# Optimization experiments

Hardware: AMD Instinct MI355X
Metric: run time of the kernel (lower is better)

Reference implementation:

```python
import jax, jax.numpy as jnp
import numpy as np

N, D_IN, D_EMB, K = 16384, 1024, 256, 1024
ALPHA, EPS = 0.01, 1e-5


def setup_inputs() -> dict:
    key = jax.random.key(0)
    ks = jax.random.split(key, 6)
    inp = jax.random.normal(ks[0], (N, D_IN), dtype=jnp.float32)
    W_send = jax.random.normal(ks[1], (D_IN, D_EMB), dtype=jnp.float32) / np.sqrt(D_IN)
    b_send = jnp.zeros((D_EMB,), dtype=jnp.float32)
    W_recv = jax.random.normal(ks[2], (D_EMB, D_IN), dtype=jnp.float32) / np.sqrt(D_EMB)
    b_recv = jnp.zeros((D_IN,), dtype=jnp.float32)
    codebook = jax.random.normal(ks[3], (K, D_EMB), dtype=jnp.float32)
    ema_vecs = codebook.copy()
    ema_size = jnp.zeros((K,), dtype=jnp.float32)
    return {"input": inp, "W_send": W_send, "b_send": b_send,
            "W_recv": W_recv, "b_recv": b_recv, "codebook": codebook,
            "ema_vecs": ema_vecs, "ema_size": ema_size}


def reference(input, W_send, b_send, W_recv, b_recv, codebook, ema_vecs, ema_size):
    sg = jax.lax.stop_gradient
    # send projection -> latent z  [N, D_EMB]
    z = input @ W_send + b_send
    # nearest-neighbor lookup: argmin_k ||e_k||^2 - 2 <z, e_k>
    sqr = jnp.sum(codebook * codebook, axis=1)          # [K]
    cov = jnp.einsum('nj,kj->nk', z, codebook)          # [N, K]
    codes = jnp.argmin(sqr - 2.0 * cov, axis=-1)        # [N] int
    # fetch embeddings (gather)
    vectors = codebook[codes]                            # [N, D_EMB]
    # mse losses, reduction='sum'
    embedding = jnp.sum((vectors - sg(z)) ** 2)
    commitment = jnp.sum((z - sg(vectors)) ** 2)
    # straight-through output
    emb_out = z + sg(vectors - z)
    # EMA accumulate (one-hot scatter == segment_sum)
    upd_vecs = jax.ops.segment_sum(z, codes, num_segments=K)              # [K, D_EMB]
    upd_size = jax.ops.segment_sum(jnp.ones((z.shape[0],), z.dtype), codes, num_segments=K)
    ema_vecs_new = ema_vecs + ALPHA * (upd_vecs - ema_vecs)
    ema_size_new = ema_size + ALPHA * (upd_size - ema_size)
    # EMA update (Laplace-smoothed centroid)
    n = jnp.sum(ema_size_new)
    coef = n / (n + K * EPS)
    size = coef * (ema_size_new + EPS)
    weight_new = ema_vecs_new / size[:, None]
    # empirical entropy of the codes in bits
    prob = jnp.bincount(codes, length=K).astype(jnp.float32) / codes.size
    ent = -jnp.sum(jnp.where(prob > 0, prob * jnp.log(prob), 0.0)) / jnp.log(2.0)
    # recv projection
    x = emb_out @ W_recv + b_recv
    return (x, codes, embedding, commitment, ent, ema_vecs_new, ema_size_new, weight_new)
```

## Files before the change

kernel.cpp:

```cpp
#include <hip/hip_runtime.h>
#include <math.h>

#define NROWS 16384
#define DIN   1024
#define DEMB  256
#define KC    1024
#define ALPHA 0.01f
#define EPSV  1e-5f
#define INV2048 4.8828125e-4f
#define CHUNK 32
#define COV_CHUNKS 8

typedef _Float16 f16;
typedef __attribute__((ext_vector_type(4)))  _Float16 f16x4;
typedef __attribute__((ext_vector_type(8)))  _Float16 f16x8;
typedef __attribute__((ext_vector_type(16))) float    f32x16;
typedef unsigned long long u64;

#define OFF_Z       0
#define OFF_R       4194304
#define OFF_SQR     5242880
#define OFF_ZH      5243904
#define OFF_ZL      7341056
#define OFF_WTH     9438208
#define OFF_WTL     9569280
#define OFF_CBH     9700352
#define OFF_CBL     9831424
#define OFF_KEYS    9962496
#define OFF_CODES   9995264
#define OFF_LIST    10011648
#define OFF_OFFS    10028032
#define OFF_UPD     10029056
#define OFF_HIST    10291200
#define OFF_CURSOR  10292224
#define OFF_LOSS    10293248
#define OFF_COUNTSF 10293264
#define OFF_SIZE    10294288

#define OUT_X      0
#define OUT_CODES  16777216
#define OUT_EMB    16793600
#define OUT_COMMIT 16793601
#define OUT_ENT    16793602
#define OUT_EMAV   16793603
#define OUT_EMAS   17055747
#define OUT_W      17056771

__device__ __forceinline__ void split_f32(float x, f16& h, f16& l) {
    h = (f16)x;
    l = (f16)((x - (float)h) * 2048.0f);
}

__global__ __launch_bounds__(256) void prep_kernel(const float* __restrict__ W_send,
                                                   const float* __restrict__ W_recv,
                                                   const float* __restrict__ cb,
                                                   float* __restrict__ ws) {
    const int b = blockIdx.x;
    const int t = threadIdx.x;
    int* wsi = (int*)ws;

    if (b < 256) {
        f16* wth = (f16*)(ws + OFF_WTH);
        f16* wtl = (f16*)(ws + OFF_WTL);
        const int n = b;
        f16x4 h4, l4;
#pragma unroll
        for (int j = 0; j < 4; ++j) {
            int k = t * 4 + j;
            float x = W_send[(size_t)k * DEMB + n];
            f16 h, l; split_f32(x, h, l);
            h4[j] = h; l4[j] = l;
        }
        *(f16x4*)&wth[(size_t)n * DIN + t * 4] = h4;
        *(f16x4*)&wtl[(size_t)n * DIN + t * 4] = l4;
    } else if (b < 512) {
        f16* cbh = (f16*)(ws + OFF_CBH);
        f16* cbl = (f16*)(ws + OFF_CBL);
        int idx = ((b - 256) * 256 + t) * 4;
        float4 v = *(const float4*)&cb[idx];
        f16x4 h4, l4;
        f16 h, l;
        split_f32(v.x, h, l); h4[0] = h; l4[0] = l;
        split_f32(v.y, h, l); h4[1] = h; l4[1] = l;
        split_f32(v.z, h, l); h4[2] = h; l4[2] = l;
        split_f32(v.w, h, l); h4[3] = h; l4[3] = l;
        *(f16x4*)&cbh[idx] = h4;
        *(f16x4*)&cbl[idx] = l4;
    } else if (b < 768) {
        f16* wrh = (f16*)(ws + OFF_ZH);
        f16* wrl = (f16*)(ws + OFF_ZH + 131072);
        const int n = (b - 512) * 4 + (t >> 6);
        const int lane = t & 63;
        f16x4 h4, l4;
#pragma unroll
        for (int j = 0; j < 4; ++j) {
            int k = lane * 4 + j;
            float x = W_recv[(size_t)k * DIN + n];
            f16 h, l; split_f32(x, h, l);
            h4[j] = h; l4[j] = l;
        }
        *(f16x4*)&wrh[(size_t)n * DEMB + lane * 4] = h4;
        *(f16x4*)&wrl[(size_t)n * DEMB + lane * 4] = l4;
    } else if (b < 1024) {
        float* sqr = ws + OFF_SQR;
        const int k = (b - 768) * 4 + (t >> 6);
        const int lane = t & 63;
        float4 v = ((const float4*)cb)[k * 64 + lane];
        float s = v.x * v.x + v.y * v.y + v.z * v.z + v.w * v.w;
        for (int off = 32; off > 0; off >>= 1) s += __shfl_down(s, off, 64);
        if (lane == 0) sqr[k] = s;
    } else if (b < 1280) {
        float4 zed = make_float4(0.f, 0.f, 0.f, 0.f);
        *(float4*)&ws[OFF_UPD + (size_t)(b - 1024) * 1024 + t * 4] = zed;
    } else if (b == 1280) {
#pragma unroll
        for (int j = 0; j < 4; ++j) {
            wsi[OFF_HIST + t * 4 + j] = 0;
            wsi[OFF_CURSOR + t * 4 + j] = 0;
        }
        if (t < 16) ws[OFF_LOSS + t] = 0.f;
    } else {
        u64* keys = (u64*)(ws + OFF_KEYS);
        keys[(b - 1281) * 256 + t] = ~0ull;
    }
}

__global__ __launch_bounds__(512) void gemm1_mfma(const float* __restrict__ in,
                                                  const f16* __restrict__ wth,
                                                  const f16* __restrict__ wtl,
                                                  const float* __restrict__ bsend,
                                                  float* __restrict__ z,
                                                  f16* __restrict__ zh,
                                                  f16* __restrict__ zl) {
    __shared__ f16 sm[2 * 2 * 2 * 128 * 64];
    const int tid = threadIdx.x;
    const int wave = tid >> 6, lane = tid & 63;
    const int half = lane >> 5, l31 = lane & 31;
    const int wrow = wave >> 2, wcol = wave & 3;

    const int L = blockIdx.x;
    const int v = L >> 3;
    const int bx = v & 1;
    const int by = (L & 7) + 8 * (v >> 1);
    const int rowBase = by * 128;
    const int colBase = bx * 128;

    const int sr  = tid >> 2;
    const int skq = tid & 3;
    const int sr7 = sr & 7;

    f32x16 accm[2] = {};
    f32x16 accx[2] = {};

    auto stageB = [&](int buf, int ks) {
#pragma unroll
        for (int i = 0; i < 4; ++i) {
            const int q  = wave * 4 + i;
            const int hl = q >> 4;
            const int c  = (q & 15) * 8 + (lane >> 3);
            const int p  = lane & 7;
            const int s  = p ^ (c & 7);
            const f16* src = (hl ? wtl : wth)
                           + (size_t)(colBase + c) * DIN + ks + s * 8;
            f16* dst = sm + buf * 32768 + 16384 + q * 512 + lane * 8;
            __builtin_amdgcn_global_load_lds(
                (const __attribute__((address_space(1))) void*)src,
                (__attribute__((address_space(3))) void*)dst, 16, 0, 0);
        }
    };

    auto loadA = [&](int ks, float4* av) {
        const float* src = &in[(size_t)(rowBase + sr) * DIN + ks + skq * 16];
#pragma unroll
        for (int j = 0; j < 4; ++j) av[j] = ((const float4*)src)[j];
    };

    auto writeA = [&](int buf, const float4* av) {
        f16* Abase = sm + buf * 32768;
#pragma unroll
        for (int q = 0; q < 2; ++q) {
            f16x8 h8, l8;
#pragma unroll
            for (int j = 0; j < 2; ++j) {
                float4 v4 = av[q * 2 + j];
                f16 h, l;
                split_f32(v4.x, h, l); h8[j * 4 + 0] = h; l8[j * 4 + 0] = l;
                split_f32(v4.y, h, l); h8[j * 4 + 1] = h; l8[j * 4 + 1] = l;
                split_f32(v4.z, h, l); h8[j * 4 + 2] = h; l8[j * 4 + 2] = l;
                split_f32(v4.w, h, l); h8[j * 4 + 3] = h; l8[j * 4 + 3] = l;
            }
            const int s = skq * 2 + q;
            const int off = sr * 64 + ((s ^ sr7) << 3);
            *(f16x8*)&Abase[off] = h8;
            *(f16x8*)&Abase[8192 + off] = l8;
        }
    };

    auto compute = [&](int buf) {
        const f16* Ah = sm + buf * 32768;
        const f16* Al = Ah + 8192;
        const f16* Bh = Ah + 16384;
        const f16* Bl = Ah + 24576;
        const int c  = wcol * 32 + l31;
        const int c7 = c & 7;
#pragma unroll
        for (int t4 = 0; t4 < 4; ++t4) {
            const int s = t4 * 2 + half;
            f16x8 a_h[2], a_l[2];
#pragma unroll
            for (int rt = 0; rt < 2; ++rt) {
                const int r = wrow * 64 + rt * 32 + l31;
                const int off = r * 64 + ((s ^ (r & 7)) << 3);
                a_h[rt] = *(const f16x8*)&Ah[off];
                a_l[rt] = *(const f16x8*)&Al[off];
            }
            const int boff = c * 64 + ((s ^ c7) << 3);
            f16x8 b_h = *(const f16x8*)&Bh[boff];
            f16x8 b_l = *(const f16x8*)&Bl[boff];
#pragma unroll
            for (int rt = 0; rt < 2; ++rt) {
                accm[rt] = __builtin_amdgcn_mfma_f32_32x32x16_f16(a_h[rt], b_h, accm[rt], 0, 0, 0);
                accx[rt] = __builtin_amdgcn_mfma_f32_32x32x16_f16(a_h[rt], b_l, accx[rt], 0, 0, 0);
                accx[rt] = __builtin_amdgcn_mfma_f32_32x32x16_f16(a_l[rt], b_h, accx[rt], 0, 0, 0);
            }
        }
    };

    stageB(0, 0);
    {
        float4 av[4];
        loadA(0, av);
        writeA(0, av);
    }
    __syncthreads();

    int cur = 0;
    for (int step = 0; step < 16; ++step) {
        float4 av[4];
        const bool pf = (step + 1) < 16;
        if (pf) {
            stageB(cur ^ 1, (step + 1) * 64);
            loadA((step + 1) * 64, av);
        }
        compute(cur);
        if (pf) writeA(cur ^ 1, av);
        __syncthreads();
        cur ^= 1;
    }

#pragma unroll
    for (int rt = 0; rt < 2; ++rt) {
        const int col = colBase + wcol * 32 + l31;
        const float bb = bsend[col];
#pragma unroll
        for (int reg = 0; reg < 16; ++reg) {
            const int row = rowBase + wrow * 64 + rt * 32 + (reg & 3) + 8 * (reg >> 2) + 4 * half;
            const float zv = accm[rt][reg] + INV2048 * accx[rt][reg] + bb;
            const size_t o = (size_t)row * DEMB + col;
            z[o] = zv;
            f16 h = (f16)zv;
            zh[o] = h;
            zl[o] = (f16)((zv - (float)h) * 2048.0f);
        }
    }
}

__global__ __launch_bounds__(256, 2) void gemm2_mfma(const f16* __restrict__ cbh,
                                                     const f16* __restrict__ cbl,
                                                     const f16* __restrict__ wrh,
                                                     const f16* __restrict__ wrl,
                                                     float* __restrict__ R) {
    __shared__ f16 sm[16384];
    const int tid = threadIdx.x;
    const int wave = tid >> 6, lane = tid & 63;
    const int half = lane >> 5, l31 = lane & 31;
    const int wr = wave >> 1, wc = wave & 1;
    const int rowBase = blockIdx.y * 64;
    const int colBase = blockIdx.x * 64;

    f32x16 accm = {}, accx = {};

    for (int step = 0; step < 4; ++step) {
        const int ks = step * 64;
        __syncthreads();
#pragma unroll
        for (int i = 0; i < 8; ++i) {
            const int q   = wave * 8 + i;
            const int arr = q >> 3;
            const int grp = q & 7;
            const int r   = grp * 8 + (lane >> 3);
            const int p   = lane & 7;
            const int s   = p ^ (r & 7);
            const f16* basep = (arr == 0) ? cbh : (arr == 1) ? cbl
                             : (arr == 2) ? wrh : wrl;
            const int rowg = ((arr >= 2) ? colBase : rowBase) + r;
            const f16* src = basep + (size_t)rowg * DEMB + ks + s * 8;
            f16* dst = sm + arr * 4096 + grp * 512;
            __builtin_amdgcn_global_load_lds(
                (const __attribute__((address_space(1))) void*)src,
                (__attribute__((address_space(3))) void*)dst, 16, 0, 0);
        }
        __syncthreads();
#pragma unroll
        for (int t = 0; t < 4; ++t) {
            const int sgi = t * 2 + half;
            const int ar = wr * 32 + l31;
            const int bc = wc * 32 + l31;
            const int aoff = ar * 64 + ((sgi ^ (ar & 7)) << 3);
            const int boff = bc * 64 + ((sgi ^ (bc & 7)) << 3);
            f16x8 a_h = *(const f16x8*)&sm[aoff];
            f16x8 a_l = *(const f16x8*)&sm[4096 + aoff];
            f16x8 b_h = *(const f16x8*)&sm[8192 + boff];
            f16x8 b_l = *(const f16x8*)&sm[12288 + boff];
            accm = __builtin_amdgcn_mfma_f32_32x32x16_f16(a_h, b_h, accm, 0, 0, 0);
            accx = __builtin_amdgcn_mfma_f32_32x32x16_f16(a_h, b_l, accx, 0, 0, 0);
            accx = __builtin_amdgcn_mfma_f32_32x32x16_f16(a_l, b_h, accx, 0, 0, 0);
        }
    }

    const int col = colBase + wc * 32 + l31;
#pragma unroll
    for (int reg = 0; reg < 16; ++reg) {
        const int row = rowBase + wr * 32 + (reg & 3) + 8 * (reg >> 2) + 4 * half;
        R[(size_t)row * DIN + col] = accm[reg] + INV2048 * accx[reg];
    }
}

__device__ __forceinline__ void cov_stage(const f16* __restrict__ cbh,
                                          const f16* __restrict__ cbl,
                                          f16* sC, int buf, int codeBase,
                                          int wave, int lane) {
#pragma unroll
    for (int i = 0; i < 8; ++i) {
        const int seg = wave * 8 + i;
        const int hl  = seg >> 4;
        const int rp  = seg & 15;
        const int r   = rp * 2 + (lane >> 5);
        const f16* src = (hl ? cbl : cbh)
                       + (size_t)(codeBase + r) * DEMB
                       + (((lane & 31) ^ r) << 3);
        f16* dst = sC + (((buf << 1) + hl) * 32 + rp * 2) * DEMB;
        __builtin_amdgcn_global_load_lds(
            (const __attribute__((address_space(1))) void*)src,
            (__attribute__((address_space(3))) void*)dst,
            16, 0, 0);
    }
}

__global__ __launch_bounds__(256, 2) void cov_mfma_kernel(const f16* __restrict__ zh,
                                                          const f16* __restrict__ zl,
                                                          const f16* __restrict__ cbh,
                                                          const f16* __restrict__ cbl,
                                                          const float* __restrict__ sqr,
                                                          u64* __restrict__ keys) {
    __shared__ f16 sC[2 * 2 * 32 * DEMB];
    const int tid = threadIdx.x;
    const int wave = tid >> 6, lane = tid & 63;
    const int half = lane >> 5, l31 = lane & 31;

    const int L = blockIdx.x;
    const int v = L >> 3;
    const int bx = v & 3;
    const int by = (L & 7) + 8 * (v >> 2);

    const int rowBase = by * 128 + wave * 32;
    const int myRow = rowBase + l31;
    const int cb0 = bx * (COV_CHUNKS * 32);

    cov_stage(cbh, cbl, sC, 0, cb0, wave, lane);

    f16x8 a_h[16], a_l[16];
#pragma unroll
    for (int t = 0; t < 16; ++t) {
        size_t o = (size_t)myRow * DEMB + t * 16 + half * 8;
        a_h[t] = *(const f16x8*)&zh[o];
        a_l[t] = *(const f16x8*)&zl[o];
    }

    float runv[16];
    int   runc[16];
#pragma unroll
    for (int r = 0; r < 16; ++r) { runv[r] = 3.4e38f; runc[r] = 0; }

    for (int cc = 0; cc < COV_CHUNKS; ++cc) {
        __syncthreads();
        if (cc + 1 < COV_CHUNKS)
            cov_stage(cbh, cbl, sC, (cc + 1) & 1, cb0 + (cc + 1) * 32, wave, lane);

        const f16* Ch = sC + ((cc & 1) * 2 + 0) * 32 * DEMB;
        const f16* Cl = sC + ((cc & 1) * 2 + 1) * 32 * DEMB;

        f32x16 accm = {};
        f32x16 accx = {};
#pragma unroll
        for (int t = 0; t < 16; ++t) {
            const int seg = t * 2 + half;
            const int p = ((seg ^ l31) << 3);
            f16x8 b_h = *(const f16x8*)&Ch[l31 * DEMB + p];
            f16x8 b_l = *(const f16x8*)&Cl[l31 * DEMB + p];
            accm = __builtin_amdgcn_mfma_f32_32x32x16_f16(a_h[t], b_h, accm, 0, 0, 0);
            accx = __builtin_amdgcn_mfma_f32_32x32x16_f16(a_h[t], b_l, accx, 0, 0, 0);
            accx = __builtin_amdgcn_mfma_f32_32x32x16_f16(a_l[t], b_h, accx, 0, 0, 0);
        }

        const int code = cb0 + cc * 32 + l31;
        const float sqv = sqr[code];
#pragma unroll
        for (int r = 0; r < 16; ++r) {
            float s = sqv - 2.0f * (accm[r] + INV2048 * accx[r]);
            if (s < runv[r]) { runv[r] = s; runc[r] = code; }
        }
    }

#pragma unroll
    for (int r = 0; r < 16; ++r) {
        float v2 = runv[r]; int ci = runc[r];
        for (int off = 16; off > 0; off >>= 1) {
            float ov = __shfl_down(v2, off, 32);
            int   oc = __shfl_down(ci, off, 32);
            if (ov < v2 || (ov == v2 && oc < ci)) { v2 = ov; ci = oc; }
        }
        if (l31 == 0) {
            int row = rowBase + (r & 3) + 8 * (r >> 2) + 4 * half;
            unsigned ub = __float_as_uint(v2);
            ub = (ub & 0x80000000u) ? ~ub : (ub | 0x80000000u);
            u64 key = ((u64)ub << 32) | (unsigned)ci;
            atomicMin(&keys[row], key);
        }
    }
}

__global__ __launch_bounds__(256) void decode_kernel(const u64* __restrict__ keys,
                                                     int* __restrict__ codes,
                                                     float* __restrict__ out_codes,
                                                     int* __restrict__ hist) {
    int r = blockIdx.x * 256 + threadIdx.x;
    int c = (int)(keys[r] & 0xFFFFFFFFull);
    codes[r] = c;
    out_codes[r] = (float)c;
    atomicAdd(&hist[c], 1);
}

__global__ __launch_bounds__(1024) void prefix_kernel(const int* __restrict__ hist,
                                                      int* __restrict__ offs,
                                                      float* __restrict__ countsf) {
    __shared__ int s[1024];
    int t = threadIdx.x;
    int v = hist[t];
    s[t] = v;
    countsf[t] = (float)v;
    __syncthreads();
    for (int d = 1; d < 1024; d <<= 1) {
        int x = (t >= d) ? s[t - d] : 0;
        __syncthreads();
        s[t] += x;
        __syncthreads();
    }
    offs[t] = s[t] - v;
}

__global__ __launch_bounds__(256) void fill_kernel(const int* __restrict__ codes,
                                                   const int* __restrict__ offs,
                                                   int* __restrict__ cursor,
                                                   int* __restrict__ list) {
    int r = blockIdx.x * 256 + threadIdx.x;
    int c = codes[r];
    int pos = offs[c] + atomicAdd(&cursor[c], 1);
    list[pos] = r;
}

__global__ __launch_bounds__(256) void upd_loss_kernel(const float* __restrict__ z,
                                                       const float* __restrict__ cb,
                                                       const int* __restrict__ list,
                                                       const int* __restrict__ codes,
                                                       float* __restrict__ upd,
                                                       float* __restrict__ loss) {
    __shared__ int srow[CHUNK];
    __shared__ int scode[CHUNK];
    const int tid = threadIdx.x;
    const int base = blockIdx.x * CHUNK;
    if (tid < CHUNK) {
        int r = list[base + tid];
        srow[tid] = r;
        scode[tid] = codes[r];
    }
    __syncthreads();

    int cur = scode[0];
    float cbv = cb[(size_t)cur * DEMB + tid];
    float acc = 0.f, lacc = 0.f;
    float zv = z[(size_t)srow[0] * DEMB + tid];
#pragma unroll 4
    for (int i = 0; i < CHUNK; ++i) {
        float znext = (i + 1 < CHUNK) ? z[(size_t)srow[i + 1] * DEMB + tid] : 0.f;
        int c = scode[i];
        if (c != cur) {
            atomicAdd(&upd[(size_t)cur * DEMB + tid], acc);
            acc = 0.f;
            cur = c;
            cbv = cb[(size_t)cur * DEMB + tid];
        }
        acc += zv;
        float d = zv - cbv;
        lacc += d * d;
        zv = znext;
    }
    atomicAdd(&upd[(size_t)cur * DEMB + tid], acc);

    __shared__ float red[256];
    red[tid] = lacc;
    __syncthreads();
    for (int s = 128; s > 0; s >>= 1) {
        if (tid < s) red[tid] += red[tid + s];
        __syncthreads();
    }
    if (tid == 0) atomicAdd(loss, red[0]);
}

__global__ __launch_bounds__(256) void recv_kernel(const float* __restrict__ R,
                                                   const float* __restrict__ brecv,
                                                   const int* __restrict__ codes,
                                                   float* __restrict__ out) {
    const int n = blockIdx.x;
    const int t = threadIdx.x;
    const int code = codes[n];
    float4 r = ((const float4*)(R + (size_t)code * DIN))[t];
    float4 b = ((const float4*)brecv)[t];
    ((float4*)(out + (size_t)n * DIN))[t] =
        make_float4(r.x + b.x, r.y + b.y, r.z + b.z, r.w + b.w);
}

__global__ __launch_bounds__(1024) void ema_small_kernel(const float* __restrict__ ema_size,
                                                         const float* __restrict__ counts,
                                                         const float* __restrict__ loss,
                                                         float* __restrict__ size_ws,
                                                         float* __restrict__ out) {
    __shared__ float rn[1024];
    __shared__ float re[1024];
    const int k = threadIdx.x;
    float c  = counts[k];
    float es = ema_size[k];
    float esn = es + ALPHA * (c - es);
    out[OUT_EMAS + k] = esn;
    float p = c * (1.0f / (float)NROWS);
    rn[k] = esn;
    re[k] = (p > 0.f) ? p * logf(p) : 0.f;
    __syncthreads();
    for (int s = 512; s > 0; s >>= 1) {
        if (k < s) { rn[k] += rn[k + s]; re[k] += re[k + s]; }
        __syncthreads();
    }
    float n = rn[0];
    float coef = n / (n + (float)KC * EPSV);
    size_ws[k] = coef * (esn + EPSV);
    if (k == 0) {
        out[OUT_ENT] = -re[0] / logf(2.0f);
        float l = loss[0];
        out[OUT_EMB] = l;
        out[OUT_COMMIT] = l;
    }
}

__global__ __launch_bounds__(256) void emav_kernel(const float* __restrict__ ema_vecs,
                                                   const float* __restrict__ upd,
                                                   const float* __restrict__ size_ws,
                                                   float* __restrict__ out) {
    int idx = blockIdx.x * 256 + threadIdx.x;
    float ev = ema_vecs[idx], uv = upd[idx];
    float evn = ev + ALPHA * (uv - ev);
    out[OUT_EMAV + idx] = evn;
    out[OUT_W + idx] = evn / size_ws[idx >> 8];
}

extern "C" void kernel_launch(void* const* d_in, const int* in_sizes, int n_in,
                              void* d_out, int out_size, void* d_ws, size_t ws_size,
                              hipStream_t stream) {
    const float* input    = (const float*)d_in[0];
    const float* W_send   = (const float*)d_in[1];
    const float* b_send   = (const float*)d_in[2];
    const float* W_recv   = (const float*)d_in[3];
    const float* b_recv   = (const float*)d_in[4];
    const float* codebook = (const float*)d_in[5];
    const float* ema_vecs = (const float*)d_in[6];
    const float* ema_size = (const float*)d_in[7];
    float* out = (float*)d_out;
    float* ws  = (float*)d_ws;
    int*   wsi = (int*)d_ws;

    f16* wth = (f16*)(ws + OFF_WTH);
    f16* wtl = (f16*)(ws + OFF_WTL);
    f16* cbh = (f16*)(ws + OFF_CBH);
    f16* cbl = (f16*)(ws + OFF_CBL);
    f16* zh  = (f16*)(ws + OFF_ZH);
    f16* zl  = (f16*)(ws + OFF_ZL);
    u64* keys = (u64*)(ws + OFF_KEYS);
    f16* wrh = (f16*)(ws + OFF_ZH);
    f16* wrl = (f16*)(ws + OFF_ZH + 131072);

    prep_kernel<<<1345, 256, 0, stream>>>(W_send, W_recv, codebook, ws);

    gemm2_mfma<<<dim3(DIN / 64, KC / 64), 256, 0, stream>>>(
        cbh, cbl, wrh, wrl, ws + OFF_R);

    gemm1_mfma<<<(DEMB / 128) * (NROWS / 128), 512, 0, stream>>>(
        input, wth, wtl, b_send, ws + OFF_Z, zh, zl);

    cov_mfma_kernel<<<(KC / (COV_CHUNKS * 32)) * (NROWS / 128), 256, 0, stream>>>(
        zh, zl, cbh, cbl, ws + OFF_SQR, keys);

    decode_kernel<<<NROWS / 256, 256, 0, stream>>>(
        keys, wsi + OFF_CODES, out + OUT_CODES, wsi + OFF_HIST);

    prefix_kernel<<<1, 1024, 0, stream>>>(
        wsi + OFF_HIST, wsi + OFF_OFFS, ws + OFF_COUNTSF);

    fill_kernel<<<NROWS / 256, 256, 0, stream>>>(
        wsi + OFF_CODES, wsi + OFF_OFFS, wsi + OFF_CURSOR, wsi + OFF_LIST);

    upd_loss_kernel<<<NROWS / CHUNK, 256, 0, stream>>>(
        ws + OFF_Z, codebook, wsi + OFF_LIST, wsi + OFF_CODES,
        ws + OFF_UPD, ws + OFF_LOSS);

    recv_kernel<<<NROWS, 256, 0, stream>>>(
        ws + OFF_R, b_recv, wsi + OFF_CODES, out + OUT_X);

    ema_small_kernel<<<1, 1024, 0, stream>>>(
        ema_size, ws + OFF_COUNTSF, ws + OFF_LOSS, ws + OFF_SIZE, out);

    emav_kernel<<<KC, 256, 0, stream>>>(
        ema_vecs, ws + OFF_UPD, ws + OFF_SIZE, out);
}
```

Before: 253.0 us.

## Double-buffer gemm2, retile cov kernel for occupancy, fuse EMA-size step into prefix

gemm2 now double-buffers its LDS stages so global loads overlap the MFMA work. The cov kernel switches to single-buffered codebook chunks and 8 code-splits per row block, with occupancy raised to 4 blocks per SM. The small EMA/entropy kernel is folded into the prefix scan. Loss outputs are written by the last block of upd_loss through an atomic ticket counter, which removes one launch but relies on that counter being reset between calls.

Measured after the change: 340.0 us. 1.34x slower.

```diff
diff --git a/kernel.cpp b/kernel.cpp
--- a/kernel.cpp
+++ b/kernel.cpp
@@ -9,7 +9,6 @@
 #define EPSV  1e-5f
 #define INV2048 4.8828125e-4f
 #define CHUNK 32
-#define COV_CHUNKS 8
 
 typedef _Float16 f16;
 typedef __attribute__((ext_vector_type(4)))  _Float16 f16x4;
@@ -34,7 +33,6 @@
 #define OFF_HIST    10291200
 #define OFF_CURSOR  10292224
 #define OFF_LOSS    10293248
-#define OFF_COUNTSF 10293264
 #define OFF_SIZE    10294288
 
 #define OUT_X      0
@@ -270,7 +268,7 @@
                                                      const f16* __restrict__ wrh,
                                                      const f16* __restrict__ wrl,
                                                      float* __restrict__ R) {
-    __shared__ f16 sm[16384];
+    __shared__ f16 sm[2 * 16384];
     const int tid = threadIdx.x;
     const int wave = tid >> 6, lane = tid & 63;
     const int half = lane >> 5, l31 = lane & 31;
@@ -280,9 +278,7 @@
 
     f32x16 accm = {}, accx = {};
 
-    for (int step = 0; step < 4; ++step) {
-        const int ks = step * 64;
-        __syncthreads();
+    auto stage = [&](int buf, int ks) {
 #pragma unroll
         for (int i = 0; i < 8; ++i) {
             const int q   = wave * 8 + i;
@@ -295,12 +291,18 @@
                              : (arr == 2) ? wrh : wrl;
             const int rowg = ((arr >= 2) ? colBase : rowBase) + r;
             const f16* src = basep + (size_t)rowg * DEMB + ks + s * 8;
-            f16* dst = sm + arr * 4096 + grp * 512;
+            f16* dst = sm + buf * 16384 + arr * 4096 + grp * 512;
             __builtin_amdgcn_global_load_lds(
                 (const __attribute__((address_space(1))) void*)src,
                 (__attribute__((address_space(3))) void*)dst, 16, 0, 0);
         }
-        __syncthreads();
+    };
+
+    stage(0, 0);
+    for (int step = 0; step < 4; ++step) {
+        __syncthreads();
+        if (step + 1 < 4) stage((step + 1) & 1, (step + 1) * 64);
+        const f16* base = sm + (step & 1) * 16384;
 #pragma unroll
         for (int t = 0; t < 4; ++t) {
             const int sgi = t * 2 + half;
@@ -308,10 +310,10 @@
             const int bc = wc * 32 + l31;
             const int aoff = ar * 64 + ((sgi ^ (ar & 7)) << 3);
             const int boff = bc * 64 + ((sgi ^ (bc & 7)) << 3);
-            f16x8 a_h = *(const f16x8*)&sm[aoff];
-            f16x8 a_l = *(const f16x8*)&sm[4096 + aoff];
-            f16x8 b_h = *(const f16x8*)&sm[8192 + boff];
-            f16x8 b_l = *(const f16x8*)&sm[12288 + boff];
+            f16x8 a_h = *(const f16x8*)&base[aoff];
+            f16x8 a_l = *(const f16x8*)&base[4096 + aoff];
+            f16x8 b_h = *(const f16x8*)&base[8192 + boff];
+            f16x8 b_l = *(const f16x8*)&base[12288 + boff];
             accm = __builtin_amdgcn_mfma_f32_32x32x16_f16(a_h, b_h, accm, 0, 0, 0);
             accx = __builtin_amdgcn_mfma_f32_32x32x16_f16(a_h, b_l, accx, 0, 0, 0);
             accx = __builtin_amdgcn_mfma_f32_32x32x16_f16(a_l, b_h, accx, 0, 0, 0);
@@ -328,7 +330,7 @@
 
 __device__ __forceinline__ void cov_stage(const f16* __restrict__ cbh,
                                           const f16* __restrict__ cbl,
-                                          f16* sC, int buf, int codeBase,
+                                          f16* sC, int codeBase,
                                           int wave, int lane) {
 #pragma unroll
     for (int i = 0; i < 8; ++i) {
@@ -339,7 +341,7 @@
         const f16* src = (hl ? cbl : cbh)
                        + (size_t)(codeBase + r) * DEMB
                        + (((lane & 31) ^ r) << 3);
-        f16* dst = sC + (((buf << 1) + hl) * 32 + rp * 2) * DEMB;
+        f16* dst = sC + (hl * 32 + rp * 2) * DEMB;
         __builtin_amdgcn_global_load_lds(
             (const __attribute__((address_space(1))) void*)src,
             (__attribute__((address_space(3))) void*)dst,
@@ -347,27 +349,25 @@
     }
 }
 
-__global__ __launch_bounds__(256, 2) void cov_mfma_kernel(const f16* __restrict__ zh,
+__global__ __launch_bounds__(256, 4) void cov_mfma_kernel(const f16* __restrict__ zh,
                                                           const f16* __restrict__ zl,
                                                           const f16* __restrict__ cbh,
                                                           const f16* __restrict__ cbl,
                                                           const float* __restrict__ sqr,
                                                           u64* __restrict__ keys) {
-    __shared__ f16 sC[2 * 2 * 32 * DEMB];
+    __shared__ f16 sC[2 * 32 * DEMB];
     const int tid = threadIdx.x;
     const int wave = tid >> 6, lane = tid & 63;
     const int half = lane >> 5, l31 = lane & 31;
 
     const int L = blockIdx.x;
     const int v = L >> 3;
-    const int bx = v & 3;
-    const int by = (L & 7) + 8 * (v >> 2);
+    const int bx = v & 7;
+    const int by = (L & 7) + 8 * (v >> 3);
 
     const int rowBase = by * 128 + wave * 32;
     const int myRow = rowBase + l31;
-    const int cb0 = bx * (COV_CHUNKS * 32);
-
-    cov_stage(cbh, cbl, sC, 0, cb0, wave, lane);
+    const int cb0 = bx * 128;
 
     f16x8 a_h[16], a_l[16];
 #pragma unroll
@@ -382,13 +382,12 @@
 #pragma unroll
     for (int r = 0; r < 16; ++r) { runv[r] = 3.4e38f; runc[r] = 0; }
 
-    for (int cc = 0; cc < COV_CHUNKS; ++cc) {
-        __syncthreads();
-        if (cc + 1 < COV_CHUNKS)
-            cov_stage(cbh, cbl, sC, (cc + 1) & 1, cb0 + (cc + 1) * 32, wave, lane);
-
-        const f16* Ch = sC + ((cc & 1) * 2 + 0) * 32 * DEMB;
-        const f16* Cl = sC + ((cc & 1) * 2 + 1) * 32 * DEMB;
+    for (int cc = 0; cc < 4; ++cc) {
+        cov_stage(cbh, cbl, sC, cb0 + cc * 32, wave, lane);
+        __syncthreads();
+
+        const f16* Ch = sC;
+        const f16* Cl = sC + 32 * DEMB;
 
         f32x16 accm = {};
         f32x16 accx = {};
@@ -410,6 +409,7 @@
             float s = sqv - 2.0f * (accm[r] + INV2048 * accx[r]);
             if (s < runv[r]) { runv[r] = s; runc[r] = code; }
         }
+        __syncthreads();
     }
 
 #pragma unroll
@@ -442,13 +442,23 @@
 }
 
 __global__ __launch_bounds__(1024) void prefix_kernel(const int* __restrict__ hist,
+                                                      const float* __restrict__ ema_size,
                                                       int* __restrict__ offs,
-                                                      float* __restrict__ countsf) {
+                                                      float* __restrict__ size_ws,
+                                                      float* __restrict__ out) {
     __shared__ int s[1024];
-    int t = threadIdx.x;
-    int v = hist[t];
+    __shared__ float rn[1024];
+    __shared__ float re[1024];
+    const int t = threadIdx.x;
+    const int v = hist[t];
     s[t] = v;
-    countsf[t] = (float)v;
+    const float c = (float)v;
+    const float es = ema_size[t];
+    const float esn = es + ALPHA * (c - es);
+    out[OUT_EMAS + t] = esn;
+    const float p = c * (1.0f / (float)NROWS);
+    rn[t] = esn;
+    re[t] = (p > 0.f) ? p * logf(p) : 0.f;
     __syncthreads();
     for (int d = 1; d < 1024; d <<= 1) {
         int x = (t >= d) ? s[t - d] : 0;
@@ -457,6 +467,14 @@
         __syncthreads();
     }
     offs[t] = s[t] - v;
+    for (int d = 512; d > 0; d >>= 1) {
+        if (t < d) { rn[t] += rn[t + d]; re[t] += re[t + d]; }
+        __syncthreads();
+    }
+    const float n = rn[0];
+    const float coef = n / (n + (float)KC * EPSV);
+    size_ws[t] = coef * (esn + EPSV);
+    if (t == 0) out[OUT_ENT] = -re[0] / logf(2.0f);
 }
 
 __global__ __launch_bounds__(256) void fill_kernel(const int* __restrict__ codes,
@@ -474,7 +492,8 @@
                                                        const int* __restrict__ list,
                                                        const int* __restrict__ codes,
                                                        float* __restrict__ upd,
-                                                       float* __restrict__ loss) {
+                                                       float* __restrict__ loss,
+                                                       float* __restrict__ out_losses) {
     __shared__ int srow[CHUNK];
     __shared__ int scode[CHUNK];
     const int tid = threadIdx.x;
@@ -514,7 +533,16 @@
         if (tid < s) red[tid] += red[tid + s];
         __syncthreads();
     }
-    if (tid == 0) atomicAdd(loss, red[0]);
+    if (tid == 0) {
+        atomicAdd(loss, red[0]);
+        __threadfence();
+        int tk = atomicAdd((int*)(loss + 8), 1);
+        if (tk == (int)gridDim.x - 1) {
+            float l = atomicAdd(loss, 0.0f);
+            out_losses[0] = l;
+            out_losses[1] = l;
+        }
+    }
 }
 
 __global__ __launch_bounds__(256) void recv_kernel(const float* __restrict__ R,
@@ -528,37 +556,6 @@
     float4 b = ((const float4*)brecv)[t];
     ((float4*)(out + (size_t)n * DIN))[t] =
         make_float4(r.x + b.x, r.y + b.y, r.z + b.z, r.w + b.w);
-}
-
-__global__ __launch_bounds__(1024) void ema_small_kernel(const float* __restrict__ ema_size,
-                                                         const float* __restrict__ counts,
-                                                         const float* __restrict__ loss,
-                                                         float* __restrict__ size_ws,
-                                                         float* __restrict__ out) {
-    __shared__ float rn[1024];
-    __shared__ float re[1024];
-    const int k = threadIdx.x;
-    float c  = counts[k];
-    float es = ema_size[k];
-    float esn = es + ALPHA * (c - es);
-    out[OUT_EMAS + k] = esn;
-    float p = c * (1.0f / (float)NROWS);
-    rn[k] = esn;
-    re[k] = (p > 0.f) ? p * logf(p) : 0.f;
-    __syncthreads();
-    for (int s = 512; s > 0; s >>= 1) {
-        if (k < s) { rn[k] += rn[k + s]; re[k] += re[k + s]; }
-        __syncthreads();
-    }
-    float n = rn[0];
-    float coef = n / (n + (float)KC * EPSV);
-    size_ws[k] = coef * (esn + EPSV);
-    if (k == 0) {
-        out[OUT_ENT] = -re[0] / logf(2.0f);
-        float l = loss[0];
-        out[OUT_EMB] = l;
-        out[OUT_COMMIT] = l;
-    }
 }
 
 __global__ __launch_bounds__(256) void emav_kernel(const float* __restrict__ ema_vecs,
@@ -605,28 +602,25 @@
     gemm1_mfma<<<(DEMB / 128) * (NROWS / 128), 512, 0, stream>>>(
         input, wth, wtl, b_send, ws + OFF_Z, zh, zl);
 
-    cov_mfma_kernel<<<(KC / (COV_CHUNKS * 32)) * (NROWS / 128), 256, 0, stream>>>(
+    cov_mfma_kernel<<<8 * (NROWS / 128), 256, 0, stream>>>(
         zh, zl, cbh, cbl, ws + OFF_SQR, keys);
 
     decode_kernel<<<NROWS / 256, 256, 0, stream>>>(
         keys, wsi + OFF_CODES, out + OUT_CODES, wsi + OFF_HIST);
 
     prefix_kernel<<<1, 1024, 0, stream>>>(
-        wsi + OFF_HIST, wsi + OFF_OFFS, ws + OFF_COUNTSF);
+        wsi + OFF_HIST, ema_size, wsi + OFF_OFFS, ws + OFF_SIZE, out);
 
     fill_kernel<<<NROWS / 256, 256, 0, stream>>>(
         wsi + OFF_CODES, wsi + OFF_OFFS, wsi + OFF_CURSOR, wsi + OFF_LIST);
 
     upd_loss_kernel<<<NROWS / CHUNK, 256, 0, stream>>>(
         ws + OFF_Z, codebook, wsi + OFF_LIST, wsi + OFF_CODES,
-        ws + OFF_UPD, ws + OFF_LOSS);
+        ws + OFF_UPD, ws + OFF_LOSS, out + OUT_EMB);
 
     recv_kernel<<<NROWS, 256, 0, stream>>>(
         ws + OFF_R, b_recv, wsi + OFF_CODES, out + OUT_X);
 
-    ema_small_kernel<<<1, 1024, 0, stream>>>(
-        ema_size, ws + OFF_COUNTSF, ws + OFF_LOSS, ws + OFF_SIZE, out);
-
     emav_kernel<<<KC, 256, 0, stream>>>(
         ema_vecs, ws + OFF_UPD, ws + OFF_SIZE, out);
 }
```
